# Kernel optimization log

Measured on AMD Instinct MI355X. Metric: run time of the kernel, lower is better.

The kernel has to match this reference:

```python
import jax, jax.numpy as jnp
import numpy as np

B, H, W, C = 4, 448, 448, 3
P = 16
G = 28            # grid = H // P
T = G * G         # 784 patches
E = 768
HD = 3072
NH = 12
DH = E // NH
L = 6
LW = 9            # local_window


def _ln(x, g, b, eps=1e-5):
    m = x.mean(-1, keepdims=True)
    v = ((x - m) ** 2).mean(-1, keepdims=True)
    return (x - m) / jnp.sqrt(v + eps) * g + b


def _mask_bias():
    # torch bool attn_mask: True = disallowed. The module sets True for LOCAL
    # neighbors (|dr|<=lw//2 and |dc|<=lw//2), so local positions are MASKED OUT.
    idx = jnp.arange(T)
    r, c = idx // G, idx % G
    local = (jnp.abs(r[:, None] - r[None, :]) <= LW // 2) & \
            (jnp.abs(c[:, None] - c[None, :]) <= LW // 2)
    return jnp.where(local, -jnp.inf, 0.0).astype(jnp.float32)  # [T, T]


def _img_to_patch(x):
    # x: [B,H,W,C] -> [B,T,C*P*P], channel-major within a patch (matches torch code)
    x = x.transpose(0, 3, 1, 2)                       # [B,C,H,W]
    x = x.reshape(B, C, G, P, G, P)
    x = x.transpose(0, 2, 4, 1, 3, 5)                 # [B,G,G,C,P,P]
    return x.reshape(B, T, C * P * P)


def _forward(x, sxr_mean, sxr_std, input_w, input_b, pos_emb,
             ln1_w, ln1_b, in_w, in_b, out_w, out_b, ln2_w, ln2_b,
             w1, b1, w2, b2, head_ln_w, head_ln_b, head_w, head_b):
    h = _img_to_patch(x) @ input_w.T + input_b        # [B,T,E]
    h = (h.reshape(B, G, G, E) + pos_emb).reshape(B, T, E)
    bias = _mask_bias()

    def block(h, prm):
        l1w, l1b, iw, ib, ow, ob, l2w, l2b, W1, B1, W2, B2 = prm
        y = _ln(h, l1w, l1b)
        qkv = y @ iw.T + ib                           # [B,T,3E]
        q, k, v = jnp.split(qkv, 3, axis=-1)
        q = q.reshape(B, T, NH, DH)
        k = k.reshape(B, T, NH, DH)
        v = v.reshape(B, T, NH, DH)
        s = jnp.einsum('bqhd,bkhd->bhqk', q, k) / jnp.sqrt(jnp.float32(DH)) + bias
        a = jax.nn.softmax(s, axis=-1)
        o = jnp.einsum('bhqk,bkhd->bqhd', a, v).reshape(B, T, E)
        h = h + o @ ow.T + ob
        y2 = _ln(h, l2w, l2b)
        m = jax.nn.gelu(y2 @ W1.T + B1, approximate=False)  # torch nn.GELU default
        h = h + m @ W2.T + B2
        return h, None

    h, _ = jax.lax.scan(block, h, (ln1_w, ln1_b, in_w, in_b, out_w, out_b,
                                   ln2_w, ln2_b, w1, b1, w2, b2))

    logits = (_ln(h, head_ln_w, head_ln_b) @ head_w.T + head_b)[..., 0]  # [B,T]
    patch_flux = jnp.clip(10.0 ** (logits * sxr_std[0] + sxr_mean[0]) - 1e-8,
                          1e-15, 1.0)
    global_flux = jnp.maximum(patch_flux.sum(axis=1, keepdims=True), 1e-15)
    return global_flux, patch_flux


def setup_inputs() -> dict:
    key = jax.random.key(0)
    ks = iter(jax.random.split(key, 16))
    def p(shape, s=0.02):
        return jax.random.normal(next(ks), shape, jnp.float32) * s
    return dict(
        x=jax.random.normal(next(ks), (B, H, W, C), jnp.float32),
        sxr_mean=jnp.array([-6.0], jnp.float32),
        sxr_std=jnp.array([1.0], jnp.float32),
        input_w=p((E, C * P * P)), input_b=jnp.zeros(E, jnp.float32),
        pos_emb=p((1, G, G, E), 1.0),
        ln1_w=jnp.ones((L, E), jnp.float32), ln1_b=jnp.zeros((L, E), jnp.float32),
        in_w=p((L, 3 * E, E)), in_b=jnp.zeros((L, 3 * E), jnp.float32),
        out_w=p((L, E, E)), out_b=jnp.zeros((L, E), jnp.float32),
        ln2_w=jnp.ones((L, E), jnp.float32), ln2_b=jnp.zeros((L, E), jnp.float32),
        w1=p((L, HD, E)), b1=jnp.zeros((L, HD), jnp.float32),
        w2=p((L, E, HD)), b2=jnp.zeros((L, E), jnp.float32),
        head_ln_w=jnp.ones(E, jnp.float32), head_ln_b=jnp.zeros(E, jnp.float32),
        head_w=p((1, E)), head_b=jnp.zeros(1, jnp.float32),
    )


def reference(x, sxr_mean, sxr_std, input_w, input_b, pos_emb,
              ln1_w, ln1_b, in_w, in_b, out_w, out_b, ln2_w, ln2_b,
              w1, b1, w2, b2, head_ln_w, head_ln_b, head_w, head_b):
    return _forward(x, sxr_mean, sxr_std, input_w, input_b, pos_emb,
                    ln1_w, ln1_b, in_w, in_b, out_w, out_b, ln2_w, ln2_b,
                    w1, b1, w2, b2, head_ln_w, head_ln_b, head_w, head_b)
```

## Files before the change

kernel.cpp:

```cpp
#include <hip/hip_runtime.h>
#include <math.h>

#define BB 4
#define TT 784
#define GG 28
#define EE 768
#define HDIM 3072
#define NHEAD 12
#define NLAYER 6
#define TTP 832

typedef short bfrag __attribute__((ext_vector_type(8)));
typedef float ffrag __attribute__((ext_vector_type(4)));

__device__ __forceinline__ unsigned short f2b(float f) {
    union { float f; unsigned u; } v; v.f = f;
    unsigned r = v.u + 0x7FFF + ((v.u >> 16) & 1);
    return (unsigned short)(r >> 16);
}

#define GLOAD_LDS16(g, l)                                                          \
    __builtin_amdgcn_global_load_lds(                                              \
        (const __attribute__((address_space(1))) void*)(g),                        \
        (__attribute__((address_space(3))) void*)(l), 16, 0, 0)

__device__ __forceinline__ float block_reduce_sum256(float v, volatile float* sb) {
    #pragma unroll
    for (int m = 1; m < 64; m <<= 1) v += __shfl_xor(v, m, 64);
    int wave = threadIdx.x >> 6;
    if ((threadIdx.x & 63) == 0) sb[wave] = v;
    __syncthreads();
    return sb[0] + sb[1] + sb[2] + sb[3];
}

__global__ __launch_bounds__(256) void cast_kernel(const float* __restrict__ s,
                                                   unsigned short* __restrict__ d, int n4) {
    int i = blockIdx.x * 256 + threadIdx.x;
    if (i >= n4) return;
    float4 v = ((const float4*)s)[i];
    ushort4 o;
    o.x = f2b(v.x); o.y = f2b(v.y); o.z = f2b(v.z); o.w = f2b(v.w);
    ((ushort4*)d)[i] = o;
}

__global__ __launch_bounds__(256) void fused_cast_kernel(const float* __restrict__ iw,
                                                         const float* __restrict__ ow,
                                                         const float* __restrict__ W1,
                                                         const float* __restrict__ W2,
                                                         unsigned short* __restrict__ dq,
                                                         unsigned short* __restrict__ doo,
                                                         unsigned short* __restrict__ d1,
                                                         unsigned short* __restrict__ d2) {
    int i = blockIdx.x * 256 + threadIdx.x;
    const float* s; unsigned short* d; int k;
    if (i < 442368)            { s = iw;  d = dq;  k = i; }
    else if (i < 589824)       { s = ow;  d = doo; k = i - 442368; }
    else if (i < 1179648)      { s = W1;  d = d1;  k = i - 589824; }
    else if (i < 1769472)      { s = W2;  d = d2;  k = i - 1179648; }
    else return;
    float4 v = ((const float4*)s)[k];
    ushort4 o;
    o.x = f2b(v.x); o.y = f2b(v.y); o.z = f2b(v.z); o.w = f2b(v.w);
    ((ushort4*)d)[k] = o;
}

__global__ __launch_bounds__(256) void patchify_kernel(const float* __restrict__ x,
                                                       unsigned short* __restrict__ P) {
    int idx = blockIdx.x * blockDim.x + threadIdx.x;
    const int total = BB * TT * EE;
    if (idx >= total) return;
    int k = idx % EE;
    int t = (idx / EE) % TT;
    int b = idx / (EE * TT);
    int c = k >> 8;
    int rem = k & 255;
    int p1 = rem >> 4;
    int p2 = rem & 15;
    int g1 = t / GG, g2 = t % GG;
    int hh = g1 * 16 + p1, ww = g2 * 16 + p2;
    P[idx] = f2b(x[((b * 448 + hh) * 448 + ww) * 3 + c]);
}

__global__ __launch_bounds__(256) void posfill_kernel(float* __restrict__ h,
                                                      const float* __restrict__ pos) {
    int idx = blockIdx.x * blockDim.x + threadIdx.x;
    const int total = BB * TT * EE;
    if (idx >= total) return;
    h[idx] = pos[idx % (TT * EE)];
}

__global__ __launch_bounds__(256) void ln_kernel(const float* __restrict__ X,
                                                 const float* __restrict__ g,
                                                 const float* __restrict__ bt,
                                                 unsigned short* __restrict__ Yb,
                                                 float* Yf) {
    __shared__ float sb1[4];
    __shared__ float sb2[4];
    int row = blockIdx.x;
    int tid = threadIdx.x;
    const float* x = X + (size_t)row * EE;
    float v0 = x[tid], v1 = x[tid + 256], v2 = x[tid + 512];
    float s = block_reduce_sum256(v0 + v1 + v2, sb1);
    float mean = s * (1.0f / 768.0f);
    float d0 = v0 - mean, d1 = v1 - mean, d2 = v2 - mean;
    __syncthreads();
    float ss = block_reduce_sum256(d0 * d0 + d1 * d1 + d2 * d2, sb2);
    float rstd = rsqrtf(ss * (1.0f / 768.0f) + 1e-5f);
    float y0 = d0 * rstd * g[tid]       + bt[tid];
    float y1 = d1 * rstd * g[tid + 256] + bt[tid + 256];
    float y2 = d2 * rstd * g[tid + 512] + bt[tid + 512];
    unsigned short* yb = Yb + (size_t)row * EE;
    yb[tid] = f2b(y0); yb[tid + 256] = f2b(y1); yb[tid + 512] = f2b(y2);
    if (Yf) {
        float* yf = Yf + (size_t)row * EE;
        yf[tid] = y0; yf[tid + 256] = y1; yf[tid + 512] = y2;
    }
}

__global__ __launch_bounds__(256) void gemm_bf16(const unsigned short* __restrict__ A,
                                                 const unsigned short* __restrict__ W,
                                                 const float* __restrict__ bias,
                                                 const float* R, float* C,
                                                 unsigned short* Cb,
                                                 int M, int N, int K, int act) {
    __shared__ unsigned short As[128 * 32];
    __shared__ unsigned short Ws[128 * 32];
    int tid = threadIdx.x;
    int wave = tid >> 6, lane = tid & 63;
    int m0 = blockIdx.y << 7, n0 = blockIdx.x << 7;
    int mh = (wave & 1) << 6, nh = (wave >> 1) << 6;

    int cl = lane & 15, qd = lane >> 4;
    int sr = lane >> 2;
    int sc = (lane & 3) << 3;

    const unsigned short* Ap[2];
    const unsigned short* Wp[2];
    unsigned short* lA[2];
    unsigned short* lW[2];
    #pragma unroll
    for (int i = 0; i < 2; i++) {
        int ar = m0 + (wave << 5) + (i << 4) + sr;
        if (ar > M - 1) ar = M - 1;
        Ap[i] = A + (size_t)ar * K + sc;
        int wr = n0 + (wave << 5) + (i << 4) + sr;
        Wp[i] = W + (size_t)wr * K + sc;
        lA[i] = &As[((wave << 5) + (i << 4)) << 5];
        lW[i] = &Ws[((wave << 5) + (i << 4)) << 5];
    }

    ffrag acc[4][4] = {};

    for (int k0 = 0; k0 < K; k0 += 32) {
        __syncthreads();
        GLOAD_LDS16(Ap[0] + k0, lA[0]);
        GLOAD_LDS16(Ap[1] + k0, lA[1]);
        GLOAD_LDS16(Wp[0] + k0, lW[0]);
        GLOAD_LDS16(Wp[1] + k0, lW[1]);
        __syncthreads();

        bfrag af[4], bfr[4];
        #pragma unroll
        for (int i = 0; i < 4; i++)
            af[i] = *(const bfrag*)&As[(((mh + (i << 4) + cl)) << 5) + (qd << 3)];
        #pragma unroll
        for (int j = 0; j < 4; j++)
            bfr[j] = *(const bfrag*)&Ws[(((nh + (j << 4) + cl)) << 5) + (qd << 3)];
        #pragma unroll
        for (int i = 0; i < 4; i++)
            #pragma unroll
            for (int j = 0; j < 4; j++)
                acc[i][j] = __builtin_amdgcn_mfma_f32_16x16x32_bf16(af[i], bfr[j], acc[i][j], 0, 0, 0);
    }

    #pragma unroll
    for (int j = 0; j < 4; j++) {
        int col = n0 + nh + (j << 4) + cl;
        float bv = bias[col];
        #pragma unroll
        for (int i = 0; i < 4; i++) {
            int row0 = m0 + mh + (i << 4) + (qd << 2);
            #pragma unroll
            for (int r = 0; r < 4; r++) {
                int row = row0 + r;
                if (row < M) {
                    float v = acc[i][j][r] + bv;
                    if (R) v += R[(size_t)row * N + col];
                    if (act) v = 0.5f * v * (1.0f + erff(v * 0.70710678118654752f));
                    if (C)  C[(size_t)row * N + col] = v;
                    if (Cb) Cb[(size_t)row * N + col] = f2b(v);
                }
            }
        }
    }
}

__global__ __launch_bounds__(256) void gemm_qkv(const unsigned short* __restrict__ A,
                                                const unsigned short* __restrict__ W,
                                                const float* __restrict__ bias,
                                                unsigned short* __restrict__ Q,
                                                unsigned short* __restrict__ Kd,
                                                unsigned short* __restrict__ vT,
                                                int M, int N, int K) {
    __shared__ unsigned short As[128 * 32];
    __shared__ unsigned short Ws[128 * 32];
    int tid = threadIdx.x;
    int wave = tid >> 6, lane = tid & 63;
    int m0 = blockIdx.y << 7, n0 = blockIdx.x << 7;
    int mh = (wave & 1) << 6, nh = (wave >> 1) << 6;

    int cl = lane & 15, qd = lane >> 4;
    int sr = lane >> 2;
    int sc = (lane & 3) << 3;

    const unsigned short* Ap[2];
    const unsigned short* Wp[2];
    unsigned short* lA[2];
    unsigned short* lW[2];
    #pragma unroll
    for (int i = 0; i < 2; i++) {
        int ar = m0 + (wave << 5) + (i << 4) + sr;
        if (ar > M - 1) ar = M - 1;
        Ap[i] = A + (size_t)ar * K + sc;
        int wr = n0 + (wave << 5) + (i << 4) + sr;
        Wp[i] = W + (size_t)wr * K + sc;
        lA[i] = &As[((wave << 5) + (i << 4)) << 5];
        lW[i] = &Ws[((wave << 5) + (i << 4)) << 5];
    }

    ffrag acc[4][4] = {};

    for (int k0 = 0; k0 < K; k0 += 32) {
        __syncthreads();
        GLOAD_LDS16(Ap[0] + k0, lA[0]);
        GLOAD_LDS16(Ap[1] + k0, lA[1]);
        GLOAD_LDS16(Wp[0] + k0, lW[0]);
        GLOAD_LDS16(Wp[1] + k0, lW[1]);
        __syncthreads();

        bfrag af[4], bfr[4];
        #pragma unroll
        for (int i = 0; i < 4; i++)
            af[i] = *(const bfrag*)&As[(((mh + (i << 4) + cl)) << 5) + (qd << 3)];
        #pragma unroll
        for (int j = 0; j < 4; j++)
            bfr[j] = *(const bfrag*)&Ws[(((nh + (j << 4) + cl)) << 5) + (qd << 3)];
        #pragma unroll
        for (int i = 0; i < 4; i++)
            #pragma unroll
            for (int j = 0; j < 4; j++)
                acc[i][j] = __builtin_amdgcn_mfma_f32_16x16x32_bf16(af[i], bfr[j], acc[i][j], 0, 0, 0);
    }

    int nb = n0 + nh;
    if (nb < 1536) {
        unsigned short* dst = (nb < 768) ? Q : Kd;
        int cb = (nb < 768) ? 0 : 768;
        #pragma unroll
        for (int j = 0; j < 4; j++) {
            int col = nb + (j << 4) + cl;
            float bv = bias[col];
            #pragma unroll
            for (int i = 0; i < 4; i++) {
                int row0 = m0 + mh + (i << 4) + (qd << 2);
                #pragma unroll
                for (int r = 0; r < 4; r++) {
                    int row = row0 + r;
                    if (row < M)
                        dst[(size_t)row * EE + col - cb] = f2b(acc[i][j][r] + bv);
                }
            }
        }
    } else {
        int hh = (nb - 1536) >> 6;
        #pragma unroll
        for (int i = 0; i < 4; i++) {
            int row0 = m0 + mh + (i << 4) + (qd << 2);
            #pragma unroll
            for (int r = 0; r < 4; r++) {
                int row = row0 + r;
                if (row < M) {
                    int b = row / TT;
                    int t = row - b * TT;
                    size_t vbase = ((size_t)(b * NHEAD + hh) * 64) * TTP + t;
                    #pragma unroll
                    for (int j = 0; j < 4; j++) {
                        int col = nb + (j << 4) + cl;
                        vT[vbase + (size_t)((j << 4) + cl) * TTP] =
                            f2b(acc[i][j][r] + bias[col]);
                    }
                }
            }
        }
    }
}

__global__ __launch_bounds__(256) void gemm_bf16_sk(const unsigned short* __restrict__ A,
                                                    const unsigned short* __restrict__ W,
                                                    const float* __restrict__ bias,
                                                    float* C,
                                                    int M, int N, int K, int KC) {
    __shared__ unsigned short As[128 * 32];
    __shared__ unsigned short Ws[128 * 32];
    int tid = threadIdx.x;
    int wave = tid >> 6, lane = tid & 63;
    int m0 = blockIdx.y << 7, n0 = blockIdx.x << 7;
    int mh = (wave & 1) << 6, nh = (wave >> 1) << 6;
    int z = blockIdx.z;
    int kbeg = z * KC;
    int kend = kbeg + KC > K ? K : kbeg + KC;

    int cl = lane & 15, qd = lane >> 4;
    int sr = lane >> 2;
    int sc = (lane & 3) << 3;

    const unsigned short* Ap[2];
    const unsigned short* Wp[2];
    unsigned short* lA[2];
    unsigned short* lW[2];
    #pragma unroll
    for (int i = 0; i < 2; i++) {
        int ar = m0 + (wave << 5) + (i << 4) + sr;
        if (ar > M - 1) ar = M - 1;
        Ap[i] = A + (size_t)ar * K + sc;
        int wr = n0 + (wave << 5) + (i << 4) + sr;
        Wp[i] = W + (size_t)wr * K + sc;
        lA[i] = &As[((wave << 5) + (i << 4)) << 5];
        lW[i] = &Ws[((wave << 5) + (i << 4)) << 5];
    }

    ffrag acc[4][4] = {};

    for (int k0 = kbeg; k0 < kend; k0 += 32) {
        __syncthreads();
        GLOAD_LDS16(Ap[0] + k0, lA[0]);
        GLOAD_LDS16(Ap[1] + k0, lA[1]);
        GLOAD_LDS16(Wp[0] + k0, lW[0]);
        GLOAD_LDS16(Wp[1] + k0, lW[1]);
        __syncthreads();

        bfrag af[4], bfr[4];
        #pragma unroll
        for (int i = 0; i < 4; i++)
            af[i] = *(const bfrag*)&As[(((mh + (i << 4) + cl)) << 5) + (qd << 3)];
        #pragma unroll
        for (int j = 0; j < 4; j++)
            bfr[j] = *(const bfrag*)&Ws[(((nh + (j << 4) + cl)) << 5) + (qd << 3)];
        #pragma unroll
        for (int i = 0; i < 4; i++)
            #pragma unroll
            for (int j = 0; j < 4; j++)
                acc[i][j] = __builtin_amdgcn_mfma_f32_16x16x32_bf16(af[i], bfr[j], acc[i][j], 0, 0, 0);
    }

    #pragma unroll
    for (int j = 0; j < 4; j++) {
        int col = n0 + nh + (j << 4) + cl;
        float bv = (z == 0) ? bias[col] : 0.0f;
        #pragma unroll
        for (int i = 0; i < 4; i++) {
            int row0 = m0 + mh + (i << 4) + (qd << 2);
            #pragma unroll
            for (int r = 0; r < 4; r++) {
                int row = row0 + r;
                if (row < M)
                    unsafeAtomicAdd(&C[(size_t)row * N + col], acc[i][j][r] + bv);
            }
        }
    }
}

#define LP 72
#define SCL2 0.18033688011112042f
__global__ __launch_bounds__(256) void attn_kernel(const unsigned short* __restrict__ Qg,
                                                   const unsigned short* __restrict__ Kg,
                                                   const unsigned short* __restrict__ vT,
                                                   unsigned short* __restrict__ O) {
    __shared__ unsigned short Ks[64 * LP];
    __shared__ unsigned short Vt[64 * LP];
    __shared__ unsigned short Pb[64 * LP];
    int tid = threadIdx.x;
    int wave = tid >> 6, lane = tid & 63;
    int cl = lane & 15, qd = lane >> 4;
    int bh = blockIdx.y;
    int b = bh / NHEAD, hh = bh % NHEAD;
    int q0 = blockIdx.x * 64;
    int qw = q0 + wave * 16;

    int qrow = qw + cl;
    if (qrow > TT - 1) qrow = TT - 1;
    const unsigned short* qb = Qg + (size_t)(b * TT + qrow) * EE + hh * 64;
    bfrag qf0 = *(const bfrag*)(qb + (qd << 3));
    bfrag qf1 = *(const bfrag*)(qb + 32 + (qd << 3));

    ffrag o_acc[4] = {};
    float m_run[4], l_run[4];
    int qg_[4], qr_[4], qc_[4];
    #pragma unroll
    for (int r = 0; r < 4; r++) {
        qg_[r] = qw + (qd << 2) + r;
        qr_[r] = qg_[r] / GG;
        qc_[r] = qg_[r] % GG;
        m_run[r] = -1e30f; l_run[r] = 0.0f;
    }

    int kr[4], kc[4];
    #pragma unroll
    for (int j = 0; j < 4; j++) {
        int kg = j * 16 + cl;
        kr[j] = kg / GG; kc[j] = kg % GG;
    }

    const unsigned short* kbase = Kg + (size_t)b * TT * EE + hh * 64;
    const unsigned short* vbase = vT + (size_t)(b * NHEAD + hh) * 64 * TTP;
    int srow = tid >> 3;
    int scol = (tid & 7) << 3;

    for (int k0 = 0; k0 < 832; k0 += 64) {
        __syncthreads();
        #pragma unroll
        for (int it = 0; it < 2; it++) {
            int row = it * 32 + srow;
            int tok = k0 + row; if (tok > TT - 1) tok = TT - 1;
            *(bfrag*)&Ks[row * LP + scol] =
                *(const bfrag*)(kbase + (size_t)tok * EE + scol);
            *(bfrag*)&Vt[row * LP + scol] =
                *(const bfrag*)(vbase + (size_t)row * TTP + k0 + scol);
        }
        __syncthreads();

        ffrag sv[4];
        #pragma unroll
        for (int j = 0; j < 4; j++) {
            bfrag kf0 = *(const bfrag*)&Ks[(j * 16 + cl) * LP + (qd << 3)];
            bfrag kf1 = *(const bfrag*)&Ks[(j * 16 + cl) * LP + 32 + (qd << 3)];
            ffrag z = {0.f, 0.f, 0.f, 0.f};
            z = __builtin_amdgcn_mfma_f32_16x16x32_bf16(qf0, kf0, z, 0, 0, 0);
            z = __builtin_amdgcn_mfma_f32_16x16x32_bf16(qf1, kf1, z, 0, 0, 0);
            sv[j] = z;
        }

        #pragma unroll
        for (int j = 0; j < 4; j++) {
            #pragma unroll
            for (int r = 0; r < 4; r++) {
                bool masked = (kr[j] > 27) ||
                              (abs(qr_[r] - kr[j]) <= 4 && abs(qc_[r] - kc[j]) <= 4);
                if (masked) sv[j][r] = -3.0e38f;
            }
        }

        #pragma unroll
        for (int r = 0; r < 4; r++) {
            float mx = fmaxf(fmaxf(sv[0][r], sv[1][r]), fmaxf(sv[2][r], sv[3][r]));
            mx = fmaxf(mx, __shfl_xor(mx, 1, 64));
            mx = fmaxf(mx, __shfl_xor(mx, 2, 64));
            mx = fmaxf(mx, __shfl_xor(mx, 4, 64));
            mx = fmaxf(mx, __shfl_xor(mx, 8, 64));
            float m_new = fmaxf(m_run[r], mx);
            float alpha = exp2f((m_run[r] - m_new) * SCL2);
            float p0 = exp2f((sv[0][r] - m_new) * SCL2);
            float p1 = exp2f((sv[1][r] - m_new) * SCL2);
            float p2 = exp2f((sv[2][r] - m_new) * SCL2);
            float p3 = exp2f((sv[3][r] - m_new) * SCL2);
            float rs = (p0 + p1) + (p2 + p3);
            rs += __shfl_xor(rs, 1, 64);
            rs += __shfl_xor(rs, 2, 64);
            rs += __shfl_xor(rs, 4, 64);
            rs += __shfl_xor(rs, 8, 64);
            l_run[r] = l_run[r] * alpha + rs;
            m_run[r] = m_new;
            #pragma unroll
            for (int t = 0; t < 4; t++) o_acc[t][r] *= alpha;
            int prow = (wave * 16 + (qd << 2) + r) * LP;
            Pb[prow + 0 * 16 + cl] = f2b(p0);
            Pb[prow + 1 * 16 + cl] = f2b(p1);
            Pb[prow + 2 * 16 + cl] = f2b(p2);
            Pb[prow + 3 * 16 + cl] = f2b(p3);
        }
        asm volatile("s_waitcnt lgkmcnt(0)" ::: "memory");

        bfrag pf0 = *(const bfrag*)&Pb[(wave * 16 + cl) * LP + (qd << 3)];
        bfrag pf1 = *(const bfrag*)&Pb[(wave * 16 + cl) * LP + 32 + (qd << 3)];
        #pragma unroll
        for (int t = 0; t < 4; t++) {
            bfrag vf0 = *(const bfrag*)&Vt[(t * 16 + cl) * LP + (qd << 3)];
            bfrag vf1 = *(const bfrag*)&Vt[(t * 16 + cl) * LP + 32 + (qd << 3)];
            o_acc[t] = __builtin_amdgcn_mfma_f32_16x16x32_bf16(pf0, vf0, o_acc[t], 0, 0, 0);
            o_acc[t] = __builtin_amdgcn_mfma_f32_16x16x32_bf16(pf1, vf1, o_acc[t], 0, 0, 0);
        }

        #pragma unroll
        for (int j = 0; j < 4; j++) {
            kc[j] += 8; kr[j] += 2;
            if (kc[j] >= GG) { kc[j] -= GG; kr[j] += 1; }
        }
    }

    #pragma unroll
    for (int r = 0; r < 4; r++) {
        if (qg_[r] < TT) {
            float inv = 1.0f / fmaxf(l_run[r], 1e-30f);
            #pragma unroll
            for (int t = 0; t < 4; t++)
                O[(size_t)(b * TT + qg_[r]) * EE + hh * 64 + t * 16 + cl] =
                    f2b(o_acc[t][r] * inv);
        }
    }
}

__global__ __launch_bounds__(256) void head_kernel(const float* __restrict__ Y,
                                                   const float* __restrict__ hw,
                                                   const float* __restrict__ hb,
                                                   const float* __restrict__ mean_,
                                                   const float* __restrict__ std_,
                                                   float* __restrict__ out) {
    __shared__ float sb[4];
    int row = blockIdx.x;
    int tid = threadIdx.x;
    const float* y = Y + (size_t)row * EE;
    float v = y[tid] * hw[tid] + y[tid + 256] * hw[tid + 256] + y[tid + 512] * hw[tid + 512];
    v = block_reduce_sum256(v, sb);
    if (tid == 0) {
        float logit = v + hb[0];
        float z = logit * std_[0] + mean_[0];
        float f = expf(z * 2.302585092994046f) - 1e-8f;
        f = fminf(fmaxf(f, 1e-15f), 1.0f);
        out[4 + row] = f;
    }
}

__global__ __launch_bounds__(256) void flux_sum_kernel(float* __restrict__ out) {
    __shared__ float sb[4];
    int b = blockIdx.x;
    int tid = threadIdx.x;
    const float* pf = out + 4 + (size_t)b * TT;
    float v = pf[tid] + pf[tid + 256] + pf[tid + 512];
    if (tid < TT - 768) v += pf[tid + 768];
    v = block_reduce_sum256(v, sb);
    if (tid == 0) out[b] = fmaxf(v, 1e-15f);
}

extern "C" void kernel_launch(void* const* d_in, const int* in_sizes, int n_in,
                              void* d_out, int out_size, void* d_ws, size_t ws_size,
                              hipStream_t stream) {
    const float* x        = (const float*)d_in[0];
    const float* sxr_mean = (const float*)d_in[1];
    const float* sxr_std  = (const float*)d_in[2];
    const float* input_w  = (const float*)d_in[3];
    const float* input_b  = (const float*)d_in[4];
    const float* pos_emb  = (const float*)d_in[5];
    const float* ln1_w    = (const float*)d_in[6];
    const float* ln1_b    = (const float*)d_in[7];
    const float* in_w     = (const float*)d_in[8];
    const float* in_b     = (const float*)d_in[9];
    const float* out_w    = (const float*)d_in[10];
    const float* out_b    = (const float*)d_in[11];
    const float* ln2_w    = (const float*)d_in[12];
    const float* ln2_b    = (const float*)d_in[13];
    const float* w1       = (const float*)d_in[14];
    const float* b1       = (const float*)d_in[15];
    const float* w2       = (const float*)d_in[16];
    const float* b2       = (const float*)d_in[17];
    const float* head_ln_w = (const float*)d_in[18];
    const float* head_ln_b = (const float*)d_in[19];
    const float* head_w   = (const float*)d_in[20];
    const float* head_b   = (const float*)d_in[21];
    float* out = (float*)d_out;

    const size_t NROW = (size_t)BB * TT;
    const size_t NE   = NROW * EE;

    float* h   = (float*)d_ws;
    float* y32 = h + NE;
    unsigned short* q_b   = (unsigned short*)(y32 + NE);
    unsigned short* k_b   = q_b + NE;
    unsigned short* vT_b  = k_b + NE;
    unsigned short* y_b   = vT_b + (size_t)BB * NHEAD * 64 * TTP;
    unsigned short* o_b   = y_b + NE;
    unsigned short* mlp_b = o_b + NE;
    unsigned short* wq_b  = mlp_b + NROW * HDIM;
    unsigned short* wo_b  = wq_b + (size_t)3 * EE * EE;
    unsigned short* w1_b  = wo_b + (size_t)EE * EE;
    unsigned short* w2_b  = w1_b + (size_t)HDIM * EE;

    const int tot = BB * TT * EE;
    const int GY = (int)((NROW + 127) / 128);

    patchify_kernel<<<(tot + 255) / 256, 256, 0, stream>>>(x, mlp_b);
    cast_kernel<<<(EE * EE / 4 + 255) / 256, 256, 0, stream>>>(input_w, wo_b, EE * EE / 4);
    posfill_kernel<<<(tot + 255) / 256, 256, 0, stream>>>(h, pos_emb);
    gemm_bf16_sk<<<dim3(EE / 128, GY, 2), 256, 0, stream>>>(
        mlp_b, wo_b, input_b, h, (int)NROW, EE, EE, 384);

    for (int l = 0; l < NLAYER; l++) {
        fused_cast_kernel<<<6912, 256, 0, stream>>>(
            in_w + (size_t)l * 3 * EE * EE, out_w + (size_t)l * EE * EE,
            w1 + (size_t)l * HDIM * EE, w2 + (size_t)l * EE * HDIM,
            wq_b, wo_b, w1_b, w2_b);

        ln_kernel<<<(int)NROW, 256, 0, stream>>>(h, ln1_w + l * EE, ln1_b + l * EE, y_b, nullptr);
        gemm_qkv<<<dim3(3 * EE / 128, GY), 256, 0, stream>>>(
            y_b, wq_b, in_b + (size_t)l * 3 * EE, q_b, k_b, vT_b,
            (int)NROW, 3 * EE, EE);
        attn_kernel<<<dim3(13, BB * NHEAD), 256, 0, stream>>>(q_b, k_b, vT_b, o_b);
        gemm_bf16_sk<<<dim3(EE / 128, GY, 2), 256, 0, stream>>>(
            o_b, wo_b, out_b + (size_t)l * EE, h, (int)NROW, EE, EE, 384);
        ln_kernel<<<(int)NROW, 256, 0, stream>>>(h, ln2_w + l * EE, ln2_b + l * EE, y_b, nullptr);
        gemm_bf16<<<dim3(HDIM / 128, GY), 256, 0, stream>>>(
            y_b, w1_b, b1 + (size_t)l * HDIM, nullptr, nullptr, mlp_b,
            (int)NROW, HDIM, EE, 1);
        gemm_bf16_sk<<<dim3(EE / 128, GY, 4), 256, 0, stream>>>(
            mlp_b, w2_b, b2 + (size_t)l * EE, h, (int)NROW, EE, HDIM, 768);
    }

    ln_kernel<<<(int)NROW, 256, 0, stream>>>(h, head_ln_w, head_ln_b, y_b, y32);
    head_kernel<<<(int)NROW, 256, 0, stream>>>(y32, head_w, head_b, sxr_mean, sxr_std, out);
    flux_sum_kernel<<<BB, 256, 0, stream>>>(out);
}
```

Baseline: 1.740 ms.

## Double-buffer GEMM LDS tiles with BK=64, XOR swizzle, and XCD-aware block remap

Factors the three GEMM kernels into a shared core that uses a two-stage LDS ping-pong with K-tile 64, so the next tile's global-to-LDS loads overlap the current tile's MFMAs. LDS rows are XOR-swizzled to avoid bank conflicts, and workgroup IDs are remapped so neighbouring tiles land on the same XCD for L2 reuse. The split-K factor for the 768-K GEMMs rises from 2 to 4. Costs are four times the LDS per block, which can lower occupancy, and more atomic adds from the deeper split-K.

Result: slower. 2.034 ms (+16.9%).

```diff
diff --git a/kernel.cpp b/kernel.cpp
--- a/kernel.cpp
+++ b/kernel.cpp
@@ -23,6 +23,19 @@
     __builtin_amdgcn_global_load_lds(                                              \
         (const __attribute__((address_space(1))) void*)(g),                        \
         (__attribute__((address_space(3))) void*)(l), 16, 0, 0)
+
+__device__ __forceinline__ void swz_bxyz(int& bx, int& by, int& bz) {
+    int gx = gridDim.x, gy = gridDim.y, gz = gridDim.z;
+    int nwg = gx * gy * gz;
+    int orig = blockIdx.x + gx * (blockIdx.y + gy * blockIdx.z);
+    int q = nwg >> 3, r = nwg & 7;
+    int xc = orig & 7, li = orig >> 3;
+    int wg = (xc < r ? xc * (q + 1) : r * (q + 1) + (xc - r) * q) + li;
+    bx = wg % gx;
+    int t = wg / gx;
+    by = t % gy;
+    bz = t / gy;
+}
 
 __device__ __forceinline__ float block_reduce_sum256(float v, volatile float* sb) {
     #pragma unroll
@@ -117,61 +130,101 @@
     }
 }
 
+__device__ __forceinline__ void gemm_core(const unsigned short* __restrict__ A,
+                                          const unsigned short* __restrict__ W,
+                                          int M, int K, int m0, int n0,
+                                          int kbeg, int nk,
+                                          unsigned short (&As)[2][8192],
+                                          unsigned short (&Ws)[2][8192],
+                                          ffrag (&acc)[4][4]) {
+    int tid = threadIdx.x;
+    int wave = tid >> 6, lane = tid & 63;
+    int cl = lane & 15, qd = lane >> 4;
+    int sr8 = lane >> 3;
+    int sbk = lane & 7;
+    int ssc = (sbk ^ sr8) << 3;
+    int mh = (wave & 1) << 6, nh = (wave >> 1) << 6;
+
+    const unsigned short* Asrc[4];
+    const unsigned short* Wsrc[4];
+    #pragma unroll
+    for (int i = 0; i < 4; i++) {
+        int ar = m0 + (wave << 5) + (i << 3) + sr8;
+        if (ar > M - 1) ar = M - 1;
+        Asrc[i] = A + (size_t)ar * K + kbeg + ssc;
+        int wr = n0 + (wave << 5) + (i << 3) + sr8;
+        Wsrc[i] = W + (size_t)wr * K + kbeg + ssc;
+    }
+    unsigned short* lAw = &As[0][0] + wave * 2048;
+    unsigned short* lWw = &Ws[0][0] + wave * 2048;
+    int fo0 = (qd ^ sbk) << 3;
+    int fo1 = ((qd ^ sbk) ^ 4) << 3;
+
+    #pragma unroll
+    for (int i = 0; i < 4; i++) {
+        GLOAD_LDS16(Asrc[i], lAw + i * 512);
+        GLOAD_LDS16(Wsrc[i], lWw + i * 512);
+    }
+    int cur = 0;
+    for (int t = 0; t < nk; ++t) {
+        if (t + 1 < nk) {
+            int kn = (t + 1) << 6;
+            unsigned short* dA = lAw + ((cur ^ 1) * 8192);
+            unsigned short* dW = lWw + ((cur ^ 1) * 8192);
+            #pragma unroll
+            for (int i = 0; i < 4; i++) {
+                GLOAD_LDS16(Asrc[i] + kn, dA + i * 512);
+                GLOAD_LDS16(Wsrc[i] + kn, dW + i * 512);
+            }
+            asm volatile("s_waitcnt vmcnt(8)" ::: "memory");
+        } else {
+            asm volatile("s_waitcnt vmcnt(0)" ::: "memory");
+        }
+        __builtin_amdgcn_s_barrier();
+        __builtin_amdgcn_sched_barrier(0);
+        const unsigned short* Ab = As[cur];
+        const unsigned short* Wb = Ws[cur];
+        bfrag af0[4], af1[4], bf0[4], bf1[4];
+        #pragma unroll
+        for (int i = 0; i < 4; i++) {
+            int ra = (mh + (i << 4) + cl) << 6;
+            int rb = (nh + (i << 4) + cl) << 6;
+            af0[i] = *(const bfrag*)&Ab[ra + fo0];
+            af1[i] = *(const bfrag*)&Ab[ra + fo1];
+            bf0[i] = *(const bfrag*)&Wb[rb + fo0];
+            bf1[i] = *(const bfrag*)&Wb[rb + fo1];
+        }
+        #pragma unroll
+        for (int i = 0; i < 4; i++)
+            #pragma unroll
+            for (int j = 0; j < 4; j++) {
+                acc[i][j] = __builtin_amdgcn_mfma_f32_16x16x32_bf16(af0[i], bf0[j], acc[i][j], 0, 0, 0);
+                acc[i][j] = __builtin_amdgcn_mfma_f32_16x16x32_bf16(af1[i], bf1[j], acc[i][j], 0, 0, 0);
+            }
+        __builtin_amdgcn_s_barrier();
+        cur ^= 1;
+    }
+}
+
 __global__ __launch_bounds__(256) void gemm_bf16(const unsigned short* __restrict__ A,
                                                  const unsigned short* __restrict__ W,
                                                  const float* __restrict__ bias,
                                                  const float* R, float* C,
                                                  unsigned short* Cb,
                                                  int M, int N, int K, int act) {
-    __shared__ unsigned short As[128 * 32];
-    __shared__ unsigned short Ws[128 * 32];
+    __shared__ unsigned short As[2][8192];
+    __shared__ unsigned short Ws[2][8192];
+    int bx, by, bz;
+    swz_bxyz(bx, by, bz);
+    int m0 = by << 7, n0 = bx << 7;
+
+    ffrag acc[4][4] = {};
+    gemm_core(A, W, M, K, m0, n0, 0, K >> 6, As, Ws, acc);
+
     int tid = threadIdx.x;
     int wave = tid >> 6, lane = tid & 63;
-    int m0 = blockIdx.y << 7, n0 = blockIdx.x << 7;
+    int cl = lane & 15, qd = lane >> 4;
     int mh = (wave & 1) << 6, nh = (wave >> 1) << 6;
-
-    int cl = lane & 15, qd = lane >> 4;
-    int sr = lane >> 2;
-    int sc = (lane & 3) << 3;
-
-    const unsigned short* Ap[2];
-    const unsigned short* Wp[2];
-    unsigned short* lA[2];
-    unsigned short* lW[2];
-    #pragma unroll
-    for (int i = 0; i < 2; i++) {
-        int ar = m0 + (wave << 5) + (i << 4) + sr;
-        if (ar > M - 1) ar = M - 1;
-        Ap[i] = A + (size_t)ar * K + sc;
-        int wr = n0 + (wave << 5) + (i << 4) + sr;
-        Wp[i] = W + (size_t)wr * K + sc;
-        lA[i] = &As[((wave << 5) + (i << 4)) << 5];
-        lW[i] = &Ws[((wave << 5) + (i << 4)) << 5];
-    }
-
-    ffrag acc[4][4] = {};
-
-    for (int k0 = 0; k0 < K; k0 += 32) {
-        __syncthreads();
-        GLOAD_LDS16(Ap[0] + k0, lA[0]);
-        GLOAD_LDS16(Ap[1] + k0, lA[1]);
-        GLOAD_LDS16(Wp[0] + k0, lW[0]);
-        GLOAD_LDS16(Wp[1] + k0, lW[1]);
-        __syncthreads();
-
-        bfrag af[4], bfr[4];
-        #pragma unroll
-        for (int i = 0; i < 4; i++)
-            af[i] = *(const bfrag*)&As[(((mh + (i << 4) + cl)) << 5) + (qd << 3)];
-        #pragma unroll
-        for (int j = 0; j < 4; j++)
-            bfr[j] = *(const bfrag*)&Ws[(((nh + (j << 4) + cl)) << 5) + (qd << 3)];
-        #pragma unroll
-        for (int i = 0; i < 4; i++)
-            #pragma unroll
-            for (int j = 0; j < 4; j++)
-                acc[i][j] = __builtin_amdgcn_mfma_f32_16x16x32_bf16(af[i], bfr[j], acc[i][j], 0, 0, 0);
-    }
 
     #pragma unroll
     for (int j = 0; j < 4; j++) {
@@ -202,63 +255,27 @@
                                                 unsigned short* __restrict__ Kd,
                                                 unsigned short* __restrict__ vT,
                                                 int M, int N, int K) {
-    __shared__ unsigned short As[128 * 32];
-    __shared__ unsigned short Ws[128 * 32];
+    __shared__ unsigned short As[2][8192];
+    __shared__ unsigned short Ws[2][8192];
+    int bx, by, bz;
+    swz_bxyz(bx, by, bz);
+    int m0 = by << 7, n0 = bx << 7;
+
+    ffrag acc[4][4] = {};
+    gemm_core(A, W, M, K, m0, n0, 0, K >> 6, As, Ws, acc);
+
     int tid = threadIdx.x;
     int wave = tid >> 6, lane = tid & 63;
-    int m0 = blockIdx.y << 7, n0 = blockIdx.x << 7;
+    int cl = lane & 15, qd = lane >> 4;
     int mh = (wave & 1) << 6, nh = (wave >> 1) << 6;
 
-    int cl = lane & 15, qd = lane >> 4;
-    int sr = lane >> 2;
-    int sc = (lane & 3) << 3;
-
-    const unsigned short* Ap[2];
-    const unsigned short* Wp[2];
-    unsigned short* lA[2];
-    unsigned short* lW[2];
-    #pragma unroll
-    for (int i = 0; i < 2; i++) {
-        int ar = m0 + (wave << 5) + (i << 4) + sr;
-        if (ar > M - 1) ar = M - 1;
-        Ap[i] = A + (size_t)ar * K + sc;
-        int wr = n0 + (wave << 5) + (i << 4) + sr;
-        Wp[i] = W + (size_t)wr * K + sc;
-        lA[i] = &As[((wave << 5) + (i << 4)) << 5];
-        lW[i] = &Ws[((wave << 5) + (i << 4)) << 5];
-    }
-
-    ffrag acc[4][4] = {};
-
-    for (int k0 = 0; k0 < K; k0 += 32) {
-        __syncthreads();
-        GLOAD_LDS16(Ap[0] + k0, lA[0]);
-        GLOAD_LDS16(Ap[1] + k0, lA[1]);
-        GLOAD_LDS16(Wp[0] + k0, lW[0]);
-        GLOAD_LDS16(Wp[1] + k0, lW[1]);
-        __syncthreads();
-
-        bfrag af[4], bfr[4];
-        #pragma unroll
-        for (int i = 0; i < 4; i++)
-            af[i] = *(const bfrag*)&As[(((mh + (i << 4) + cl)) << 5) + (qd << 3)];
-        #pragma unroll
-        for (int j = 0; j < 4; j++)
-            bfr[j] = *(const bfrag*)&Ws[(((nh + (j << 4) + cl)) << 5) + (qd << 3)];
-        #pragma unroll
-        for (int i = 0; i < 4; i++)
-            #pragma unroll
-            for (int j = 0; j < 4; j++)
-                acc[i][j] = __builtin_amdgcn_mfma_f32_16x16x32_bf16(af[i], bfr[j], acc[i][j], 0, 0, 0);
-    }
-
-    int nb = n0 + nh;
-    if (nb < 1536) {
-        unsigned short* dst = (nb < 768) ? Q : Kd;
-        int cb = (nb < 768) ? 0 : 768;
+    int ncb = n0 + nh;
+    if (ncb < 1536) {
+        unsigned short* dst = (ncb < 768) ? Q : Kd;
+        int cb = (ncb < 768) ? 0 : 768;
         #pragma unroll
         for (int j = 0; j < 4; j++) {
-            int col = nb + (j << 4) + cl;
+            int col = ncb + (j << 4) + cl;
             float bv = bias[col];
             #pragma unroll
             for (int i = 0; i < 4; i++) {
@@ -272,7 +289,7 @@
             }
         }
     } else {
-        int hh = (nb - 1536) >> 6;
+        int hh = (ncb - 1536) >> 6;
         #pragma unroll
         for (int i = 0; i < 4; i++) {
             int row0 = m0 + mh + (i << 4) + (qd << 2);
@@ -285,7 +302,7 @@
                     size_t vbase = ((size_t)(b * NHEAD + hh) * 64) * TTP + t;
                     #pragma unroll
                     for (int j = 0; j < 4; j++) {
-                        int col = nb + (j << 4) + cl;
+                        int col = ncb + (j << 4) + cl;
                         vT[vbase + (size_t)((j << 4) + cl) * TTP] =
                             f2b(acc[i][j][r] + bias[col]);
                     }
@@ -300,58 +317,22 @@
                                                     const float* __restrict__ bias,
                                                     float* C,
                                                     int M, int N, int K, int KC) {
-    __shared__ unsigned short As[128 * 32];
-    __shared__ unsigned short Ws[128 * 32];
+    __shared__ unsigned short As[2][8192];
+    __shared__ unsigned short Ws[2][8192];
+    int bx, by, bz;
+    swz_bxyz(bx, by, bz);
+    int m0 = by << 7, n0 = bx << 7;
+    int z = bz;
+    int kbeg = z * KC;
+    int kc2 = (kbeg + KC > K) ? (K - kbeg) : KC;
+
+    ffrag acc[4][4] = {};
+    gemm_core(A, W, M, K, m0, n0, kbeg, kc2 >> 6, As, Ws, acc);
+
     int tid = threadIdx.x;
     int wave = tid >> 6, lane = tid & 63;
-    int m0 = blockIdx.y << 7, n0 = blockIdx.x << 7;
+    int cl = lane & 15, qd = lane >> 4;
     int mh = (wave & 1) << 6, nh = (wave >> 1) << 6;
-    int z = blockIdx.z;
-    int kbeg = z * KC;
-    int kend = kbeg + KC > K ? K : kbeg + KC;
-
-    int cl = lane & 15, qd = lane >> 4;
-    int sr = lane >> 2;
-    int sc = (lane & 3) << 3;
-
-    const unsigned short* Ap[2];
-    const unsigned short* Wp[2];
-    unsigned short* lA[2];
-    unsigned short* lW[2];
-    #pragma unroll
-    for (int i = 0; i < 2; i++) {
-        int ar = m0 + (wave << 5) + (i << 4) + sr;
-        if (ar > M - 1) ar = M - 1;
-        Ap[i] = A + (size_t)ar * K + sc;
-        int wr = n0 + (wave << 5) + (i << 4) + sr;
-        Wp[i] = W + (size_t)wr * K + sc;
-        lA[i] = &As[((wave << 5) + (i << 4)) << 5];
-        lW[i] = &Ws[((wave << 5) + (i << 4)) << 5];
-    }
-
-    ffrag acc[4][4] = {};
-
-    for (int k0 = kbeg; k0 < kend; k0 += 32) {
-        __syncthreads();
-        GLOAD_LDS16(Ap[0] + k0, lA[0]);
-        GLOAD_LDS16(Ap[1] + k0, lA[1]);
-        GLOAD_LDS16(Wp[0] + k0, lW[0]);
-        GLOAD_LDS16(Wp[1] + k0, lW[1]);
-        __syncthreads();
-
-        bfrag af[4], bfr[4];
-        #pragma unroll
-        for (int i = 0; i < 4; i++)
-            af[i] = *(const bfrag*)&As[(((mh + (i << 4) + cl)) << 5) + (qd << 3)];
-        #pragma unroll
-        for (int j = 0; j < 4; j++)
-            bfr[j] = *(const bfrag*)&Ws[(((nh + (j << 4) + cl)) << 5) + (qd << 3)];
-        #pragma unroll
-        for (int i = 0; i < 4; i++)
-            #pragma unroll
-            for (int j = 0; j < 4; j++)
-                acc[i][j] = __builtin_amdgcn_mfma_f32_16x16x32_bf16(af[i], bfr[j], acc[i][j], 0, 0, 0);
-    }
 
     #pragma unroll
     for (int j = 0; j < 4; j++) {
@@ -590,8 +571,8 @@
     patchify_kernel<<<(tot + 255) / 256, 256, 0, stream>>>(x, mlp_b);
     cast_kernel<<<(EE * EE / 4 + 255) / 256, 256, 0, stream>>>(input_w, wo_b, EE * EE / 4);
     posfill_kernel<<<(tot + 255) / 256, 256, 0, stream>>>(h, pos_emb);
-    gemm_bf16_sk<<<dim3(EE / 128, GY, 2), 256, 0, stream>>>(
-        mlp_b, wo_b, input_b, h, (int)NROW, EE, EE, 384);
+    gemm_bf16_sk<<<dim3(EE / 128, GY, 4), 256, 0, stream>>>(
+        mlp_b, wo_b, input_b, h, (int)NROW, EE, EE, 192);
 
     for (int l = 0; l < NLAYER; l++) {
         fused_cast_kernel<<<6912, 256, 0, stream>>>(
@@ -604,8 +585,8 @@
             y_b, wq_b, in_b + (size_t)l * 3 * EE, q_b, k_b, vT_b,
             (int)NROW, 3 * EE, EE);
         attn_kernel<<<dim3(13, BB * NHEAD), 256, 0, stream>>>(q_b, k_b, vT_b, o_b);
-        gemm_bf16_sk<<<dim3(EE / 128, GY, 2), 256, 0, stream>>>(
-            o_b, wo_b, out_b + (size_t)l * EE, h, (int)NROW, EE, EE, 384);
+        gemm_bf16_sk<<<dim3(EE / 128, GY, 4), 256, 0, stream>>>(
+            o_b, wo_b, out_b + (size_t)l * EE, h, (int)NROW, EE, EE, 192);
         ln_kernel<<<(int)NROW, 256, 0, stream>>>(h, ln2_w + l * EE, ln2_b + l * EE, y_b, nullptr);
         gemm_bf16<<<dim3(HDIM / 128, GY), 256, 0, stream>>>(
             y_b, w1_b, b1 + (size_t)l * HDIM, nullptr, nullptr, mlp_b,
```
